# Performance work log

Hardware: AMD Instinct MI355X
Metric: run time of the kernel (lower is better)

The kernel has to match this reference:

```python
import jax, jax.numpy as jnp
import numpy as np

B, S, HID = 1, 2048, 2880
H, KV, D = 64, 8, 64
WINDOW = 128
SCALE = D ** -0.5
NEG_INF = jnp.float32(-1e30)


def _rope_cos_sin():
    # realistic RoPE tables over full head_dim (HF rotate_half convention)
    inv_freq = 1.0 / (10000.0 ** (np.arange(0, D, 2, dtype=np.float32) / D))
    t = np.arange(S, dtype=np.float32)
    freqs = np.outer(t, inv_freq)                      # [S, D/2]
    emb = np.concatenate([freqs, freqs], axis=-1)      # [S, D]
    return jnp.asarray(np.cos(emb))[None], jnp.asarray(np.sin(emb))[None]


def setup_inputs() -> dict:
    key = jax.random.key(0)
    ks = jax.random.split(key, 10)
    cos, sin = _rope_cos_sin()
    sd = lambda fan_in: 1.0 / np.sqrt(fan_in)
    return {
        "hidden_states": jax.random.normal(ks[0], (B, S, HID), jnp.float32),
        "cos": cos, "sin": sin,
        "Wq": jax.random.normal(ks[1], (HID, H * D), jnp.float32) * sd(HID),
        "bq": jax.random.normal(ks[2], (H * D,), jnp.float32) * 0.02,
        "Wk": jax.random.normal(ks[3], (HID, KV * D), jnp.float32) * sd(HID),
        "bk": jax.random.normal(ks[4], (KV * D,), jnp.float32) * 0.02,
        "Wv": jax.random.normal(ks[5], (HID, KV * D), jnp.float32) * sd(HID),
        "bv": jax.random.normal(ks[6], (KV * D,), jnp.float32) * 0.02,
        "Wo": jax.random.normal(ks[7], (H * D, HID), jnp.float32) * sd(H * D),
        "bo": jax.random.normal(ks[8], (HID,), jnp.float32) * 0.02,
        "sinks": jax.random.normal(ks[9], (H,), jnp.float32),
    }


def _rotate_half(x):
    x1, x2 = jnp.split(x, 2, axis=-1)
    return jnp.concatenate([-x2, x1], axis=-1)


def _forward(hidden_states, cos, sin, Wq, bq, Wk, bk, Wv, bv, Wo, bo, sinks):
    q = (hidden_states @ Wq + bq).reshape(B, S, H, D)
    k = (hidden_states @ Wk + bk).reshape(B, S, KV, D)
    v = (hidden_states @ Wv + bv).reshape(B, S, KV, D)
    # RoPE with explicit cos/sin, unsqueeze at head dim (bsnd layout)
    c, s = cos[:, :, None, :], sin[:, :, None, :]
    q = q * c + _rotate_half(q) * s
    k = k * c + _rotate_half(k) * s
    # GQA: expand kv heads to match query heads
    k = jnp.repeat(k, H // KV, axis=2)
    v = jnp.repeat(v, H // KV, axis=2)
    scores = jnp.einsum("bqhd,bkhd->bhqk", q, k) * SCALE  # [B,H,S,S]
    i = jnp.arange(S)[:, None]
    j = jnp.arange(S)[None, :]
    allowed = (j <= i) & (j > i - WINDOW)                  # causal + sliding window
    scores = jnp.where(allowed, scores, NEG_INF)
    # sink-augmented softmax: sinks act as an extra logit per head, dropped after norm
    m = jnp.maximum(scores.max(axis=-1), sinks[None, :, None])  # [B,H,S]
    p = jnp.exp(scores - m[..., None])                      # [B,H,S,S]
    denom = p.sum(axis=-1) + jnp.exp(sinks[None, :, None] - m)  # [B,H,S]
    attn = jnp.einsum("bhqk,bkhd->bqhd", p, v) / denom.transpose(0, 2, 1)[..., None]
    return attn.reshape(B, S, H * D) @ Wo + bo


def reference(hidden_states, cos, sin, Wq, bq, Wk, bk, Wv, bv, Wo, bo, sinks):
    return _forward(hidden_states, cos, sin, Wq, bq, Wk, bk, Wv, bv, Wo, bo, sinks)
```

## Files before the change

kernel.cpp:

```cpp
#include <hip/hip_runtime.h>

typedef unsigned short u16;
typedef __bf16 bf16x8 __attribute__((ext_vector_type(8)));
typedef float f32x4 __attribute__((ext_vector_type(4)));

constexpr int SEQ = 2048;
constexpr int HIDN = 2880;
constexpr int NHEAD = 64;
constexpr int NKVH = 8;
constexpr int DHEAD = 64;
constexpr int NQKV = 5120;
constexpr float SCALE = 0.125f;
constexpr float NEG_INF = -1e30f;

__device__ __forceinline__ u16 f2bf(float f) {
  unsigned int u = __builtin_bit_cast(unsigned int, f);
  u += 0x7FFFu + ((u >> 16) & 1u);
  return (u16)(u >> 16);
}
__device__ __forceinline__ float bf2f(u16 h) {
  unsigned int u = ((unsigned int)h) << 16;
  return __builtin_bit_cast(float, u);
}
__device__ __forceinline__ void async_load16(const void* g, void* l) {
  __builtin_amdgcn_global_load_lds(
      (const __attribute__((address_space(1))) unsigned int*)g,
      (__attribute__((address_space(3))) unsigned int*)l, 16, 0, 0);
}

__global__ __launch_bounds__(256) void conv_f2b(const float* __restrict__ in,
                                                u16* __restrict__ out, long n4) {
  long i = (long)blockIdx.x * 256 + threadIdx.x;
  if (i >= n4) return;
  float4 v = ((const float4*)in)[i];
  u16 o0 = f2bf(v.x), o1 = f2bf(v.y), o2 = f2bf(v.z), o3 = f2bf(v.w);
  out[i * 4 + 0] = o0; out[i * 4 + 1] = o1; out[i * 4 + 2] = o2; out[i * 4 + 3] = o3;
}

__global__ __launch_bounds__(256) void transpose_f2b(const float* __restrict__ in,
                                                     u16* __restrict__ out,
                                                     int R, int C, int ostride) {
  __shared__ float tile[32][33];
  int c0 = blockIdx.x * 32, r0 = blockIdx.y * 32;
  int tx = threadIdx.x & 31, ty = threadIdx.x >> 5;
#pragma unroll
  for (int i = 0; i < 32; i += 8)
    tile[ty + i][tx] = in[(long)(r0 + ty + i) * C + c0 + tx];
  __syncthreads();
#pragma unroll
  for (int i = 0; i < 32; i += 8)
    out[(long)(c0 + ty + i) * ostride + r0 + tx] = f2bf(tile[tx][ty + i]);
}

__global__ __launch_bounds__(256) void concat_bias(const float* bq, const float* bk,
                                                   const float* bv, float* out) {
  int t = blockIdx.x * 256 + threadIdx.x;
  if (t < 4096) out[t] = bq[t];
  else if (t < 4608) out[t] = bk[t - 4096];
  else if (t < 5120) out[t] = bv[t - 4608];
}

template <bool OUT_BF16>
__global__ __launch_bounds__(256, 2) void gemm_bt(const u16* __restrict__ A,
                                                  const u16* __restrict__ B,
                                                  const float* __restrict__ bias,
                                                  void* __restrict__ Cout,
                                                  int M, int N, int K) {
  __shared__ u16 As[128 * 32];
  __shared__ u16 Bs[128 * 32];
  const int tid = threadIdx.x;
  const int wid = tid >> 6, lane = tid & 63;
  const int lr = lane & 15, lk = lane >> 4;
  const int wm = wid >> 1, wn = wid & 1;
  const long brow = (long)blockIdx.x * 128;
  const long bcol = (long)blockIdx.y * 128;

  f32x4 acc[4][4] = {};
  const int nk = K >> 5;
  for (int kt = 0; kt < nk; ++kt) {
    const long k0 = (long)kt * 32;
#pragma unroll
    for (int i = 0; i < 2; ++i) {
      int c = wid * 128 + i * 64 + lane;
      int row = c >> 2, sub = c & 3;
      async_load16(A + (brow + row) * K + k0 + sub * 8, ((char*)As) + c * 16);
      async_load16(B + (bcol + row) * K + k0 + sub * 8, ((char*)Bs) + c * 16);
    }
    __syncthreads();
    bf16x8 af[4], bfr[4];
#pragma unroll
    for (int m = 0; m < 4; ++m)
      af[m] = *(const bf16x8*)&As[(wm * 64 + m * 16 + lr) * 32 + lk * 8];
#pragma unroll
    for (int n = 0; n < 4; ++n)
      bfr[n] = *(const bf16x8*)&Bs[(wn * 64 + n * 16 + lr) * 32 + lk * 8];
#pragma unroll
    for (int m = 0; m < 4; ++m)
#pragma unroll
      for (int n = 0; n < 4; ++n)
        acc[m][n] = __builtin_amdgcn_mfma_f32_16x16x32_bf16(af[m], bfr[n], acc[m][n], 0, 0, 0);
    __syncthreads();
  }
#pragma unroll
  for (int m = 0; m < 4; ++m) {
    long row = brow + wm * 64 + m * 16 + lk * 4;
#pragma unroll
    for (int n = 0; n < 4; ++n) {
      long col = bcol + wn * 64 + n * 16 + lr;
      if (col < N) {
        float bv = bias[col];
#pragma unroll
        for (int r = 0; r < 4; ++r) {
          float v = acc[m][n][r] + bv;
          if (OUT_BF16) ((u16*)Cout)[(row + r) * (long)N + col] = f2bf(v);
          else          ((float*)Cout)[(row + r) * (long)N + col] = v;
        }
      }
    }
  }
}

__global__ __launch_bounds__(256) void rope_kernel(u16* __restrict__ QKV,
                                                   const float* __restrict__ cosb,
                                                   const float* __restrict__ sinb) {
  long idx = (long)blockIdx.x * 256 + threadIdx.x;
  if (idx >= (long)SEQ * 72 * 32) return;
  int d = idx & 31;
  int h = (int)((idx >> 5) % 72);
  int s = (int)(idx / (72 * 32));
  int col = (h < 64) ? h * 64 : 4096 + (h - 64) * 64;
  u16* p = QKV + (long)s * NQKV + col;
  float x1 = bf2f(p[d]), x2 = bf2f(p[d + 32]);
  float c = cosb[s * 64 + d], sn = sinb[s * 64 + d];
  p[d]      = f2bf(x1 * c - x2 * sn);
  p[d + 32] = f2bf(x2 * c + x1 * sn);
}

__global__ __launch_bounds__(256, 1) void attn_kernel(const u16* __restrict__ QKV,
                                                      const float* __restrict__ sinks,
                                                      u16* __restrict__ Oa) {
  __shared__ u16 Ks[64 * 64];
  __shared__ u16 Vt[64 * 64];
  __shared__ u16 Ps[4][64 * 72];
  const int tid = threadIdx.x, wid = tid >> 6, lane = tid & 63;
  const int lr = lane & 15, lk = lane >> 4;
  const int i0 = blockIdx.x * 64;
  const int h = blockIdx.y * 4 + wid;
  const int g = h >> 3;

  bf16x8 qf[4][2];
#pragma unroll
  for (int m = 0; m < 4; ++m)
#pragma unroll
    for (int kc = 0; kc < 2; ++kc)
      qf[m][kc] = *(const bf16x8*)&QKV[(long)(i0 + m * 16 + lr) * NQKV + h * 64 + kc * 32 + lk * 8];

  const float sinkh = sinks[h];
  float mrun[4][4], lrun[4][4];
  f32x4 oacc[4][4] = {};
#pragma unroll
  for (int m = 0; m < 4; ++m)
#pragma unroll
    for (int r = 0; r < 4; ++r) { mrun[m][r] = sinkh; lrun[m][r] = 0.f; }

  const int jb0 = (i0 >= 128) ? (i0 - 128) : 0;
  for (int jb = jb0; jb <= i0; jb += 64) {
#pragma unroll
    for (int i = 0; i < 2; ++i) {
      int c = wid * 128 + i * 64 + lane;
      int row = c >> 3, sub = c & 7;
      async_load16(QKV + (long)(jb + row) * NQKV + 4096 + g * 64 + sub * 8,
                   ((char*)Ks) + c * 16);
    }
    {
      int j = tid >> 2, d0 = (tid & 3) * 16;
      const u16* vp = QKV + (long)(jb + j) * NQKV + 4608 + g * 64 + d0;
      u16 tmp[16];
      *(int4*)(tmp)     = *(const int4*)(vp);
      *(int4*)(tmp + 8) = *(const int4*)(vp + 8);
#pragma unroll
      for (int e = 0; e < 16; ++e) Vt[(d0 + e) * 64 + j] = tmp[e];
    }
    __syncthreads();

    f32x4 sf[4][4] = {};
#pragma unroll
    for (int kc = 0; kc < 2; ++kc) {
      bf16x8 kf[4];
#pragma unroll
      for (int cf = 0; cf < 4; ++cf)
        kf[cf] = *(const bf16x8*)&Ks[(cf * 16 + lr) * 64 + kc * 32 + lk * 8];
#pragma unroll
      for (int m = 0; m < 4; ++m)
#pragma unroll
        for (int cf = 0; cf < 4; ++cf)
          sf[m][cf] = __builtin_amdgcn_mfma_f32_16x16x32_bf16(qf[m][kc], kf[cf], sf[m][cf], 0, 0, 0);
    }

#pragma unroll
    for (int m = 0; m < 4; ++m) {
      float rmax[4];
#pragma unroll
      for (int r = 0; r < 4; ++r) {
        int i = i0 + m * 16 + lk * 4 + r;
        float mx = NEG_INF;
#pragma unroll
        for (int cf = 0; cf < 4; ++cf) {
          int j = jb + cf * 16 + lr;
          float v = sf[m][cf][r] * SCALE;
          bool ok = (j <= i) && (j > i - 128);
          v = ok ? v : NEG_INF;
          sf[m][cf][r] = v;
          mx = fmaxf(mx, v);
        }
#pragma unroll
        for (int off = 1; off < 16; off <<= 1) mx = fmaxf(mx, __shfl_xor(mx, off, 64));
        rmax[r] = mx;
      }
#pragma unroll
      for (int r = 0; r < 4; ++r) {
        float mnew = fmaxf(mrun[m][r], rmax[r]);
        float corr = __expf(mrun[m][r] - mnew);
        mrun[m][r] = mnew;
        float rsum = 0.f;
#pragma unroll
        for (int cf = 0; cf < 4; ++cf) {
          float p = __expf(sf[m][cf][r] - mnew);
          sf[m][cf][r] = p;
          rsum += p;
        }
#pragma unroll
        for (int off = 1; off < 16; off <<= 1) rsum += __shfl_xor(rsum, off, 64);
        lrun[m][r] = lrun[m][r] * corr + rsum;
#pragma unroll
        for (int dn = 0; dn < 4; ++dn) oacc[m][dn][r] *= corr;
      }
    }

#pragma unroll
    for (int m = 0; m < 4; ++m)
#pragma unroll
      for (int cf = 0; cf < 4; ++cf)
#pragma unroll
        for (int r = 0; r < 4; ++r)
          Ps[wid][(m * 16 + lk * 4 + r) * 72 + cf * 16 + lr] = f2bf(sf[m][cf][r]);
    __syncthreads();

#pragma unroll
    for (int kc = 0; kc < 2; ++kc) {
      bf16x8 pf[4], vf[4];
#pragma unroll
      for (int m = 0; m < 4; ++m)
        pf[m] = *(const bf16x8*)&Ps[wid][(m * 16 + lr) * 72 + kc * 32 + lk * 8];
#pragma unroll
      for (int dn = 0; dn < 4; ++dn)
        vf[dn] = *(const bf16x8*)&Vt[(dn * 16 + lr) * 64 + kc * 32 + lk * 8];
#pragma unroll
      for (int m = 0; m < 4; ++m)
#pragma unroll
        for (int dn = 0; dn < 4; ++dn)
          oacc[m][dn] = __builtin_amdgcn_mfma_f32_16x16x32_bf16(pf[m], vf[dn], oacc[m][dn], 0, 0, 0);
    }
    __syncthreads();
  }

#pragma unroll
  for (int m = 0; m < 4; ++m)
#pragma unroll
    for (int r = 0; r < 4; ++r) {
      float denom = lrun[m][r] + __expf(sinkh - mrun[m][r]);
      float inv = 1.f / denom;
      long row = i0 + m * 16 + lk * 4 + r;
#pragma unroll
      for (int dn = 0; dn < 4; ++dn)
        Oa[row * 4096 + h * 64 + dn * 16 + lr] = f2bf(oacc[m][dn][r] * inv);
    }
}

extern "C" void kernel_launch(void* const* d_in, const int* in_sizes, int n_in,
                              void* d_out, int out_size, void* d_ws, size_t ws_size,
                              hipStream_t stream) {
  const float* X    = (const float*)d_in[0];
  const float* cosb = (const float*)d_in[1];
  const float* sinb = (const float*)d_in[2];
  const float* Wq   = (const float*)d_in[3];
  const float* bq   = (const float*)d_in[4];
  const float* Wk   = (const float*)d_in[5];
  const float* bk   = (const float*)d_in[6];
  const float* Wv   = (const float*)d_in[7];
  const float* bv   = (const float*)d_in[8];
  const float* Wo   = (const float*)d_in[9];
  const float* bo   = (const float*)d_in[10];
  const float* sinks = (const float*)d_in[11];

  char* ws = (char*)d_ws;
  size_t off = 0;
  auto alloc = [&](size_t bytes) -> void* {
    void* p = ws + off;
    off += (bytes + 255) & ~(size_t)255;
    return p;
  };
  u16*   Xb    = (u16*)alloc((size_t)SEQ * HIDN * 2);
  u16*   Wqkv  = (u16*)alloc((size_t)NQKV * HIDN * 2);
  u16*   Wot   = (u16*)alloc((size_t)2944 * 4096 * 2);
  float* bqkv  = (float*)alloc((size_t)NQKV * 4);
  u16*   QKV   = (u16*)alloc((size_t)SEQ * NQKV * 2);
  u16*   Ab    = (u16*)alloc((size_t)SEQ * 4096 * 2);
  (void)ws_size; (void)in_sizes; (void)n_in; (void)out_size;

  conv_f2b<<<(SEQ * HIDN / 4 + 255) / 256, 256, 0, stream>>>(X, Xb, (long)SEQ * HIDN / 4);
  transpose_f2b<<<dim3(4096 / 32, HIDN / 32), 256, 0, stream>>>(Wq, Wqkv, HIDN, 4096, HIDN);
  transpose_f2b<<<dim3(512 / 32, HIDN / 32), 256, 0, stream>>>(Wk, Wqkv + (size_t)4096 * HIDN, HIDN, 512, HIDN);
  transpose_f2b<<<dim3(512 / 32, HIDN / 32), 256, 0, stream>>>(Wv, Wqkv + (size_t)4608 * HIDN, HIDN, 512, HIDN);
  transpose_f2b<<<dim3(HIDN / 32, 4096 / 32), 256, 0, stream>>>(Wo, Wot, 4096, HIDN, 4096);
  concat_bias<<<(NQKV + 255) / 256, 256, 0, stream>>>(bq, bk, bv, bqkv);
  gemm_bt<true><<<dim3(SEQ / 128, NQKV / 128), 256, 0, stream>>>(Xb, Wqkv, bqkv, QKV, SEQ, NQKV, HIDN);
  rope_kernel<<<(int)(((long)SEQ * 72 * 32 + 255) / 256), 256, 0, stream>>>(QKV, cosb, sinb);
  attn_kernel<<<dim3(SEQ / 64, NHEAD / 4), 256, 0, stream>>>(QKV, sinks, Ab);
  gemm_bt<false><<<dim3(SEQ / 128, (HIDN + 127) / 128), 256, 0, stream>>>(Ab, Wot, bo, d_out, SEQ, HIDN, 4096);
}
```

Baseline: 267.4 us.

## Triple-buffer GEMM loads with XCD-aware block swizzle and swizzled LDS layouts

The GEMM becomes a three-stage async LDS pipeline with explicit vmcnt waits and a single barrier per k-step, so global loads overlap the MFMA work. Blocks are remapped so neighbouring tiles land on the same XCD for L2 reuse, and the LDS layout is XOR-swizzled to avoid bank conflicts. The attention kernel gets XOR-swizzled K and V-transpose layouts, a cheaper packed V transpose store, and s_setprio around its MFMA sections. The extra buffers raise LDS use, and the hand-written waitcnt counts depend on the exact number of loads issued per stage.

```diff
diff --git a/kernel.cpp b/kernel.cpp
--- a/kernel.cpp
+++ b/kernel.cpp
@@ -6,12 +6,14 @@
 
 constexpr int SEQ = 2048;
 constexpr int HIDN = 2880;
-constexpr int NHEAD = 64;
-constexpr int NKVH = 8;
-constexpr int DHEAD = 64;
 constexpr int NQKV = 5120;
 constexpr float SCALE = 0.125f;
 constexpr float NEG_INF = -1e30f;
+
+#define ASM_VMCNT4()  asm volatile("s_waitcnt vmcnt(4)" ::: "memory")
+#define ASM_VMCNT0()  asm volatile("s_waitcnt vmcnt(0)" ::: "memory")
+#define ASM_LGKM0()   asm volatile("s_waitcnt lgkmcnt(0)" ::: "memory")
+#define ASM_BARRIER() asm volatile("s_barrier" ::: "memory")
 
 __device__ __forceinline__ u16 f2bf(float f) {
   unsigned int u = __builtin_bit_cast(unsigned int, f);
@@ -61,46 +63,84 @@
 }
 
 template <bool OUT_BF16>
-__global__ __launch_bounds__(256, 2) void gemm_bt(const u16* __restrict__ A,
-                                                  const u16* __restrict__ B,
-                                                  const float* __restrict__ bias,
-                                                  void* __restrict__ Cout,
-                                                  int M, int N, int K) {
-  __shared__ u16 As[128 * 32];
-  __shared__ u16 Bs[128 * 32];
+__global__ __launch_bounds__(256, 3) void gemm_pipe(const u16* __restrict__ A,
+                                                    const u16* __restrict__ B,
+                                                    const float* __restrict__ bias,
+                                                    void* __restrict__ Cout,
+                                                    int M, int N, int K) {
+  __shared__ u16 As[3][128 * 32];
+  __shared__ u16 Bs[3][128 * 32];
   const int tid = threadIdx.x;
   const int wid = tid >> 6, lane = tid & 63;
   const int lr = lane & 15, lk = lane >> 4;
   const int wm = wid >> 1, wn = wid & 1;
-  const long brow = (long)blockIdx.x * 128;
-  const long bcol = (long)blockIdx.y * 128;
+
+  const int gm = gridDim.x;
+  int nwg = gm * gridDim.y;
+  int bid = blockIdx.y * gm + blockIdx.x;
+  int q8 = nwg >> 3, r8 = nwg & 7;
+  int xcd = bid & 7, seq = bid >> 3;
+  int swz = (xcd < r8 ? xcd * (q8 + 1) : r8 * (q8 + 1) + (xcd - r8) * q8) + seq;
+  const long brow = (long)(swz % gm) * 128;
+  const long bcol = (long)(swz / gm) * 128;
+
+  const int c0 = wid * 128 + lane;
+  const int c1 = c0 + 64;
+  const int r0s = c0 >> 2, k0s = ((c0 & 3) ^ ((r0s >> 1) & 3)) * 8;
+  const int r1s = c1 >> 2, k1s = ((c1 & 3) ^ ((r1s >> 1) & 3)) * 8;
+  const u16* Asrc0 = A + (brow + r0s) * (long)K + k0s;
+  const u16* Asrc1 = A + (brow + r1s) * (long)K + k1s;
+  const u16* Bsrc0 = B + (bcol + r0s) * (long)K + k0s;
+  const u16* Bsrc1 = B + (bcol + r1s) * (long)K + k1s;
+  char* AsB = (char*)&As[0][0];
+  char* BsB = (char*)&Bs[0][0];
+
+  auto stage = [&](int kt, int bufi) {
+    long ko = (long)kt * 32;
+    char* la = AsB + bufi * 8192;
+    char* lb = BsB + bufi * 8192;
+    async_load16(Asrc0 + ko, la + c0 * 16);
+    async_load16(Bsrc0 + ko, lb + c0 * 16);
+    async_load16(Asrc1 + ko, la + c1 * 16);
+    async_load16(Bsrc1 + ko, lb + c1 * 16);
+  };
+
+  const int phys = (lk ^ ((lr >> 1) & 3)) << 4;
+  const int aoff0 = (wm * 64 + lr) * 64 + phys;
+  const int boff0 = (wn * 64 + lr) * 64 + phys;
 
   f32x4 acc[4][4] = {};
   const int nk = K >> 5;
+
+  stage(0, 0);
+  if (nk > 1) stage(1, 1);
+
+  int b = 0, sb = 2;
   for (int kt = 0; kt < nk; ++kt) {
-    const long k0 = (long)kt * 32;
-#pragma unroll
-    for (int i = 0; i < 2; ++i) {
-      int c = wid * 128 + i * 64 + lane;
-      int row = c >> 2, sub = c & 3;
-      async_load16(A + (brow + row) * K + k0 + sub * 8, ((char*)As) + c * 16);
-      async_load16(B + (bcol + row) * K + k0 + sub * 8, ((char*)Bs) + c * 16);
-    }
-    __syncthreads();
+    if (kt + 1 < nk) { ASM_VMCNT4(); } else { ASM_VMCNT0(); }
+    ASM_BARRIER();
+    __builtin_amdgcn_sched_barrier(0);
+    if (kt + 2 < nk) stage(kt + 2, sb);
+    char* Ab_ = AsB + b * 8192;
+    char* Bb_ = BsB + b * 8192;
     bf16x8 af[4], bfr[4];
 #pragma unroll
-    for (int m = 0; m < 4; ++m)
-      af[m] = *(const bf16x8*)&As[(wm * 64 + m * 16 + lr) * 32 + lk * 8];
-#pragma unroll
-    for (int n = 0; n < 4; ++n)
-      bfr[n] = *(const bf16x8*)&Bs[(wn * 64 + n * 16 + lr) * 32 + lk * 8];
+    for (int m = 0; m < 4; ++m) af[m] = *(const bf16x8*)(Ab_ + aoff0 + m * 1024);
+#pragma unroll
+    for (int n = 0; n < 4; ++n) bfr[n] = *(const bf16x8*)(Bb_ + boff0 + n * 1024);
+    ASM_LGKM0();
+    __builtin_amdgcn_sched_barrier(0);
+    __builtin_amdgcn_s_setprio(1);
 #pragma unroll
     for (int m = 0; m < 4; ++m)
 #pragma unroll
       for (int n = 0; n < 4; ++n)
         acc[m][n] = __builtin_amdgcn_mfma_f32_16x16x32_bf16(af[m], bfr[n], acc[m][n], 0, 0, 0);
-    __syncthreads();
+    __builtin_amdgcn_s_setprio(0);
+    b = (b == 2) ? 0 : b + 1;
+    sb = (sb == 2) ? 0 : sb + 1;
   }
+
 #pragma unroll
   for (int m = 0; m < 4; ++m) {
     long row = brow + wm * 64 + m * 16 + lk * 4;
@@ -168,34 +208,45 @@
 #pragma unroll
     for (int i = 0; i < 2; ++i) {
       int c = wid * 128 + i * 64 + lane;
-      int row = c >> 3, sub = c & 7;
-      async_load16(QKV + (long)(jb + row) * NQKV + 4096 + g * 64 + sub * 8,
+      int row = c >> 3, sp = c & 7;
+      int ssrc = sp ^ (row & 7);
+      async_load16(QKV + (long)(jb + row) * NQKV + 4096 + g * 64 + ssrc * 8,
                    ((char*)Ks) + c * 16);
     }
     {
-      int j = tid >> 2, d0 = (tid & 3) * 16;
-      const u16* vp = QKV + (long)(jb + j) * NQKV + 4608 + g * 64 + d0;
-      u16 tmp[16];
-      *(int4*)(tmp)     = *(const int4*)(vp);
-      *(int4*)(tmp + 8) = *(const int4*)(vp + 8);
-#pragma unroll
-      for (int e = 0; e < 16; ++e) Vt[(d0 + e) * 64 + j] = tmp[e];
+      int j0 = (tid & 31) * 2, d0 = (tid >> 5) * 8;
+      const u16* vp = QKV + (long)(jb + j0) * NQKV + 4608 + g * 64 + d0;
+      int4 rv0 = *(const int4*)vp;
+      int4 rv1 = *(const int4*)(vp + NQKV);
+      const u16* a0 = (const u16*)&rv0;
+      const u16* a1 = (const u16*)&rv1;
+#pragma unroll
+      for (int e = 0; e < 8; ++e) {
+        int d = d0 + e;
+        unsigned val = (unsigned)a0[e] | ((unsigned)a1[e] << 16);
+        int byt = d * 128 + ((((j0 >> 3) ^ (d & 7)) << 4)) + ((j0 & 7) * 2);
+        *(unsigned*)((char*)Vt + byt) = val;
+      }
     }
     __syncthreads();
 
     f32x4 sf[4][4] = {};
+    __builtin_amdgcn_s_setprio(1);
 #pragma unroll
     for (int kc = 0; kc < 2; ++kc) {
       bf16x8 kf[4];
 #pragma unroll
-      for (int cf = 0; cf < 4; ++cf)
-        kf[cf] = *(const bf16x8*)&Ks[(cf * 16 + lr) * 64 + kc * 32 + lk * 8];
+      for (int cf = 0; cf < 4; ++cf) {
+        int row = cf * 16 + lr;
+        kf[cf] = *(const bf16x8*)((const char*)Ks + row * 128 + (((kc * 4 + lk) ^ (lr & 7)) << 4));
+      }
 #pragma unroll
       for (int m = 0; m < 4; ++m)
 #pragma unroll
         for (int cf = 0; cf < 4; ++cf)
           sf[m][cf] = __builtin_amdgcn_mfma_f32_16x16x32_bf16(qf[m][kc], kf[cf], sf[m][cf], 0, 0, 0);
     }
+    __builtin_amdgcn_s_setprio(0);
 
 #pragma unroll
     for (int m = 0; m < 4; ++m) {
@@ -246,6 +297,7 @@
           Ps[wid][(m * 16 + lk * 4 + r) * 72 + cf * 16 + lr] = f2bf(sf[m][cf][r]);
     __syncthreads();
 
+    __builtin_amdgcn_s_setprio(1);
 #pragma unroll
     for (int kc = 0; kc < 2; ++kc) {
       bf16x8 pf[4], vf[4];
@@ -253,14 +305,17 @@
       for (int m = 0; m < 4; ++m)
         pf[m] = *(const bf16x8*)&Ps[wid][(m * 16 + lr) * 72 + kc * 32 + lk * 8];
 #pragma unroll
-      for (int dn = 0; dn < 4; ++dn)
-        vf[dn] = *(const bf16x8*)&Vt[(dn * 16 + lr) * 64 + kc * 32 + lk * 8];
+      for (int dn = 0; dn < 4; ++dn) {
+        int row = dn * 16 + lr;
+        vf[dn] = *(const bf16x8*)((const char*)Vt + row * 128 + (((kc * 4 + lk) ^ (lr & 7)) << 4));
+      }
 #pragma unroll
       for (int m = 0; m < 4; ++m)
 #pragma unroll
         for (int dn = 0; dn < 4; ++dn)
           oacc[m][dn] = __builtin_amdgcn_mfma_f32_16x16x32_bf16(pf[m], vf[dn], oacc[m][dn], 0, 0, 0);
     }
+    __builtin_amdgcn_s_setprio(0);
     __syncthreads();
   }
 
@@ -314,8 +369,8 @@
   transpose_f2b<<<dim3(512 / 32, HIDN / 32), 256, 0, stream>>>(Wv, Wqkv + (size_t)4608 * HIDN, HIDN, 512, HIDN);
   transpose_f2b<<<dim3(HIDN / 32, 4096 / 32), 256, 0, stream>>>(Wo, Wot, 4096, HIDN, 4096);
   concat_bias<<<(NQKV + 255) / 256, 256, 0, stream>>>(bq, bk, bv, bqkv);
-  gemm_bt<true><<<dim3(SEQ / 128, NQKV / 128), 256, 0, stream>>>(Xb, Wqkv, bqkv, QKV, SEQ, NQKV, HIDN);
+  gemm_pipe<true><<<dim3(SEQ / 128, NQKV / 128), 256, 0, stream>>>(Xb, Wqkv, bqkv, QKV, SEQ, NQKV, HIDN);
   rope_kernel<<<(int)(((long)SEQ * 72 * 32 + 255) / 256), 256, 0, stream>>>(QKV, cosb, sinb);
-  attn_kernel<<<dim3(SEQ / 64, NHEAD / 4), 256, 0, stream>>>(QKV, sinks, Ab);
-  gemm_bt<false><<<dim3(SEQ / 128, (HIDN + 127) / 128), 256, 0, stream>>>(Ab, Wot, bo, d_out, SEQ, HIDN, 4096);
-}
+  attn_kernel<<<dim3(SEQ / 64, 64 / 4), 256, 0, stream>>>(QKV, sinks, Ab);
+  gemm_pipe<false><<<dim3(SEQ / 128, (HIDN + 127) / 128), 256, 0, stream>>>(Ab, Wot, bo, d_out, SEQ, HIDN, 4096);
+}
```

New measurement: 259.7 us. 2.9% less time.
